# Performance work log

Hardware: AMD Instinct MI355X
Metric: run time of the kernel (lower is better)

## Reference

```python
import jax, jax.numpy as jnp
import numpy as np

DIM = 192
HEADS = 4
B, H, W = 4, 128, 128


def _dwconv3(x, w):
    # depthwise 3x3, padding=1: w has shape [C, 1, 3, 3], groups = C
    return jax.lax.conv_general_dilated(
        x, w, window_strides=(1, 1), padding='SAME',
        feature_group_count=x.shape[1],
        dimension_numbers=('NCHW', 'OIHW', 'NCHW'))


def _conv1x1(x, w):
    # w: [O, C] (squeezed 1x1 kernel), bias=False
    return jnp.einsum('bchw,oc->bohw', x, w)


def _l2norm(t):
    # torch F.normalize(dim=-1), eps=1e-12
    n = jnp.sqrt(jnp.sum(t * t, axis=-1, keepdims=True))
    return t / jnp.maximum(n, 1e-12)


def setup_inputs() -> dict:
    key = jax.random.key(0)
    ks = jax.random.split(key, 12)
    s = 0.05
    return {
        'x': jax.random.normal(ks[0], (B, DIM, H, W), jnp.float32),
        'x_hidden': jax.random.normal(ks[1], (B, DIM, H, W), jnp.float32),
        'qkv_w': jax.random.normal(ks[2], (3 * DIM, DIM), jnp.float32) * s,
        'qkv_dw_w': jax.random.normal(ks[3], (3 * DIM, 1, 3, 3), jnp.float32) * s,
        'q_mut_w': jax.random.normal(ks[4], (DIM, DIM), jnp.float32) * s,
        'q_mut_dw_w': jax.random.normal(ks[5], (DIM, 1, 3, 3), jnp.float32) * s,
        'kv_mut_w': jax.random.normal(ks[6], (2 * DIM, DIM), jnp.float32) * s,
        'kv_mut_dw_w': jax.random.normal(ks[7], (2 * DIM, 1, 3, 3), jnp.float32) * s,
        'proj_w': jax.random.normal(ks[8], (DIM, 2 * DIM), jnp.float32) * s,
        'temperature': jnp.ones((HEADS, 1, 1), jnp.float32),
        'temperature_mut': jnp.ones((HEADS, 1, 1), jnp.float32),
    }


def reference(x, x_hidden, qkv_w, qkv_dw_w, q_mut_w, q_mut_dw_w,
              kv_mut_w, kv_mut_dw_w, proj_w, temperature, temperature_mut):
    b, c, h, w = x.shape
    heads = HEADS

    qkv = _dwconv3(_conv1x1(x, qkv_w), qkv_dw_w)
    q, k, v = jnp.split(qkv, 3, axis=1)
    q_mut = _dwconv3(_conv1x1(x, q_mut_w), q_mut_dw_w)
    kv_mut = _dwconv3(_conv1x1(x_hidden, kv_mut_w), kv_mut_dw_w)
    k_mut, v_mut = jnp.split(kv_mut, 2, axis=1)

    def rs(t):  # b (head c') h w -> b head c' (h w)
        return t.reshape(b, heads, c // heads, h * w)

    q, k, v = rs(q), rs(k), rs(v)
    q_mut, k_mut, v_mut = rs(q_mut), rs(k_mut), rs(v_mut)

    q, k = _l2norm(q), _l2norm(k)
    q_mut, k_mut = _l2norm(q_mut), _l2norm(k_mut)

    # channel-wise (transposed) attention: [b, head, c', c']
    attn = jax.nn.softmax(
        jnp.einsum('bhcn,bhdn->bhcd', q, k) * temperature, axis=-1)
    cross = jax.nn.softmax(
        jnp.einsum('bhcn,bhdn->bhcd', q_mut, k_mut) * temperature_mut, axis=-1)

    out = jnp.einsum('bhcd,bhdn->bhcn', attn, v).reshape(b, c, h, w)
    out_mut = jnp.einsum('bhcd,bhdn->bhcn', cross, v_mut).reshape(b, c, h, w)

    return _conv1x1(jnp.concatenate((out, out_mut), axis=1), proj_w)
```

## Files before the change

### kernel.cpp

```cpp
#include <hip/hip_runtime.h>
#include <hip/hip_bf16.h>

typedef __hip_bfloat16 bf16;
using short8  = __attribute__((ext_vector_type(8))) short;
using float4_ = __attribute__((ext_vector_type(4))) float;

#define B_    4
#define C_    192
#define NN    16384
#define HEADS 4
#define CHD   48
#define TOT   1152

__device__ __forceinline__ float b2f(bf16 v) { return __bfloat162float(v); }
__device__ __forceinline__ float s2f(short s) {
    return __uint_as_float(((unsigned)(unsigned short)s) << 16);
}

__global__ __launch_bounds__(256) void kprep_w(
    const float* __restrict__ qkv_w, const float* __restrict__ qm_w,
    const float* __restrict__ kvm_w, bf16* __restrict__ Wb)
{
    int i = blockIdx.x * 256 + threadIdx.x;
    if (i >= TOT * C_) return;
    int r = i / C_, c = i % C_;
    float v = (r < 576) ? qkv_w[r * C_ + c]
            : (r < 768) ? qm_w[(r - 576) * C_ + c]
                        : kvm_w[(r - 768) * C_ + c];
    Wb[i] = __float2bfloat16(v);
}

__global__ __launch_bounds__(256) void kprep_x(
    const float* __restrict__ x, const float* __restrict__ xh,
    int p, bf16* __restrict__ Xt)
{
    const int pb = blockIdx.z >> 1, src = blockIdx.z & 1;
    const int b = p * 2 + pb;
    const float* in = (src == 0 ? x : xh) + (size_t)b * C_ * NN;
    bf16* outp = Xt + ((size_t)pb * 2 + src) * NN * C_;
    const int n0 = blockIdx.x * 64, c0 = blockIdx.y * 64;
    __shared__ float t[64][65];
    const int tid = threadIdx.x;

    #pragma unroll
    for (int it = 0; it < 4; ++it) {
        const int id = it * 256 + tid;
        const int c = id >> 4, i4 = (id & 15) * 4;
        const float4_ v = *(const float4_*)&in[(size_t)(c0 + c) * NN + n0 + i4];
        t[c][i4 + 0] = v[0]; t[c][i4 + 1] = v[1];
        t[c][i4 + 2] = v[2]; t[c][i4 + 3] = v[3];
    }
    __syncthreads();

    #pragma unroll
    for (int it = 0; it < 2; ++it) {
        const int id = it * 256 + tid;
        const int n = id >> 3, j8 = (id & 7) * 8;
        short8 sv;
        #pragma unroll
        for (int k = 0; k < 8; ++k) {
            bf16 h = __float2bfloat16(t[j8 + k][n]);
            sv[k] = *reinterpret_cast<short*>(&h);
        }
        *(short8*)&outp[(size_t)(n0 + n) * C_ + c0 + j8] = sv;
    }
}

__global__ __launch_bounds__(256) void kgemm(
    const bf16* __restrict__ Wb, const bf16* __restrict__ Xt,
    bf16* __restrict__ Y)
{
    const int nt0 = blockIdx.x * 128;
    const int mt0 = blockIdx.y * 64;
    const int pb  = blockIdx.z;
    const int tid = threadIdx.x;
    const bf16* Xs = Xt + ((size_t)pb * 2 + (mt0 >= 768 ? 1 : 0)) * NN * C_;
    bf16* Yp = Y + (size_t)pb * TOT * NN;

    __shared__ short sA[64][72];
    __shared__ short sB[128][72];

    const int wave = tid >> 6, lane = tid & 63;
    const int mw = (wave & 1) * 32, nw = (wave >> 1) * 64;
    const int lm = lane & 15, lq = lane >> 4;

    float4_ acc[2][4];
    #pragma unroll
    for (int i = 0; i < 2; ++i)
        #pragma unroll
        for (int j = 0; j < 4; ++j)
            acc[i][j] = (float4_){0.f, 0.f, 0.f, 0.f};

    for (int kc = 0; kc < 192; kc += 64) {
        __syncthreads();
        {
            int r = tid >> 3, c8 = (tid & 7) * 8;
            #pragma unroll
            for (int it = 0; it < 2; ++it, r += 32)
                *(short8*)&sA[r][c8] =
                    *(const short8*)&Wb[(size_t)(mt0 + r) * C_ + kc + c8];
        }
        {
            int r = tid >> 3, c8 = (tid & 7) * 8;
            #pragma unroll
            for (int it = 0; it < 4; ++it, r += 32)
                *(short8*)&sB[r][c8] =
                    *(const short8*)&Xs[(size_t)(nt0 + r) * C_ + kc + c8];
        }
        __syncthreads();
        #pragma unroll
        for (int kk = 0; kk < 64; kk += 32) {
            short8 af[2], bfr[4];
            const int ko = kk + lq * 8;
            #pragma unroll
            for (int i = 0; i < 2; ++i)
                af[i] = *(const short8*)&sA[mw + i * 16 + lm][ko];
            #pragma unroll
            for (int j = 0; j < 4; ++j)
                bfr[j] = *(const short8*)&sB[nw + j * 16 + lm][ko];
            #pragma unroll
            for (int i = 0; i < 2; ++i)
                #pragma unroll
                for (int j = 0; j < 4; ++j)
                    acc[i][j] = __builtin_amdgcn_mfma_f32_16x16x32_bf16(
                        af[i], bfr[j], acc[i][j], 0, 0, 0);
        }
    }
    #pragma unroll
    for (int i = 0; i < 2; ++i)
        #pragma unroll
        for (int j = 0; j < 4; ++j) {
            const int n = nt0 + nw + j * 16 + lm;
            #pragma unroll
            for (int r = 0; r < 4; ++r) {
                const int m = mt0 + mw + i * 16 + lq * 4 + r;
                Yp[(size_t)m * NN + n] = __float2bfloat16(acc[i][j][r]);
            }
        }
}

__device__ __forceinline__ void kdw_load_row(
    float* r, const bf16* __restrict__ Yc, int row, int x0, int lane)
{
    float f[8];
    if (row >= 0 && row <= 127) {
        short8 v = *(const short8*)(Yc + row * 128 + x0);
        #pragma unroll
        for (int i = 0; i < 8; ++i) f[i] = s2f(v[i]);
    } else {
        #pragma unroll
        for (int i = 0; i < 8; ++i) f[i] = 0.f;
    }
    const float lf = __shfl(f[7], lane - 1);
    const float rf = __shfl(f[0], lane + 1);
    r[0] = (x0 > 0)   ? lf : 0.f;
    r[9] = (x0 < 120) ? rf : 0.f;
    #pragma unroll
    for (int i = 0; i < 8; ++i) r[i + 1] = f[i];
}

__global__ __launch_bounds__(256) void kdw(
    const bf16* __restrict__ Y,
    const float* __restrict__ qkv_dw, const float* __restrict__ qm_dw,
    const float* __restrict__ kvm_dw, int p, bf16* __restrict__ QT,
    float* __restrict__ nrmsq)
{
    const int ch  = blockIdx.x;
    const int pb  = blockIdx.z;
    const int b   = p * 2 + pb;
    const int tid = threadIdx.x;
    const int tx = tid & 15, ty = tid >> 4;
    const int lane = tid & 63;
    const int x0 = tx * 8;
    const int y0 = blockIdx.y * 64 + ty * 4;

    const float* dwp = (ch < 576) ? qkv_dw + (size_t)ch * 9
                     : (ch < 768) ? qm_dw + (size_t)(ch - 576) * 9
                                  : kvm_dw + (size_t)(ch - 768) * 9;
    float w[9];
    #pragma unroll
    for (int i = 0; i < 9; ++i) w[i] = dwp[i];

    const bf16* Yc = Y + ((size_t)pb * TOT + ch) * NN;
    bf16* qout = QT + ((size_t)b * TOT + ch) * NN;

    float r0[10], r1[10], r2[10];
    kdw_load_row(r0, Yc, y0 - 1, x0, lane);
    kdw_load_row(r1, Yc, y0,     x0, lane);

    float ssq = 0.f;
    #pragma unroll
    for (int yy = 0; yy < 4; ++yy) {
        kdw_load_row(r2, Yc, y0 + yy + 1, x0, lane);
        short8 sv;
        #pragma unroll
        for (int xx = 0; xx < 8; ++xx) {
            float s = w[0] * r0[xx] + w[1] * r0[xx + 1] + w[2] * r0[xx + 2]
                    + w[3] * r1[xx] + w[4] * r1[xx + 1] + w[5] * r1[xx + 2]
                    + w[6] * r2[xx] + w[7] * r2[xx + 1] + w[8] * r2[xx + 2];
            ssq += s * s;
            bf16 h = __float2bfloat16(s);
            sv[xx] = *reinterpret_cast<short*>(&h);
        }
        *(short8*)&qout[(size_t)(y0 + yy) * 128 + x0] = sv;
        #pragma unroll
        for (int i = 0; i < 10; ++i) { r0[i] = r1[i]; r1[i] = r2[i]; }
    }

    int cls = -1, ci = 0;
    if (ch < 192)                    { cls = 0; ci = ch; }
    else if (ch < 384)               { cls = 1; ci = ch - 192; }
    else if (ch >= 576 && ch < 768)  { cls = 2; ci = ch - 576; }
    else if (ch >= 768 && ch < 960)  { cls = 3; ci = ch - 768; }
    if (cls >= 0) {
        #pragma unroll
        for (int off = 32; off > 0; off >>= 1) ssq += __shfl_down(ssq, off);
        __shared__ float red[4];
        if ((tid & 63) == 0) red[tid >> 6] = ssq;
        __syncthreads();
        if (tid == 0)
            atomicAdd(&nrmsq[(b * 4 + cls) * 192 + ci],
                      red[0] + red[1] + red[2] + red[3]);
    }
}

__global__ __launch_bounds__(256) void k3_mfma(
    const bf16* __restrict__ QT, float* __restrict__ Gpart)
{
    const int chunk = blockIdx.x;
    const int t = blockIdx.y >> 2, h = blockIdx.y & 3;
    const int b = blockIdx.z;
    const int qch = (t == 0 ? 0 : 576) + h * CHD;
    const int kch = (t == 0 ? 192 : 768) + h * CHD;
    const bf16* qp = QT + ((size_t)b * TOT + qch) * NN;
    const bf16* kp = QT + ((size_t)b * TOT + kch) * NN;

    const int tid = threadIdx.x;
    const int wave = tid >> 6, lane = tid & 63;
    const int lm = lane & 15, lq = lane >> 4;
    const int n0 = chunk * 512 + wave * 128;

    float4_ acc[3][3];
    #pragma unroll
    for (int i = 0; i < 3; ++i)
        #pragma unroll
        for (int j = 0; j < 3; ++j)
            acc[i][j] = (float4_){0.f, 0.f, 0.f, 0.f};

    #pragma unroll
    for (int kk = 0; kk < 128; kk += 32) {
        short8 af[3], bfr[3];
        const int ko = n0 + kk + lq * 8;
        #pragma unroll
        for (int i = 0; i < 3; ++i)
            af[i] = *(const short8*)&qp[(size_t)(i * 16 + lm) * NN + ko];
        #pragma unroll
        for (int j = 0; j < 3; ++j)
            bfr[j] = *(const short8*)&kp[(size_t)(j * 16 + lm) * NN + ko];
        #pragma unroll
        for (int i = 0; i < 3; ++i)
            #pragma unroll
            for (int j = 0; j < 3; ++j)
                acc[i][j] = __builtin_amdgcn_mfma_f32_16x16x32_bf16(
                    af[i], bfr[j], acc[i][j], 0, 0, 0);
    }

    __shared__ float sW[4][48 * 49];
    #pragma unroll
    for (int i = 0; i < 3; ++i)
        #pragma unroll
        for (int j = 0; j < 3; ++j)
            #pragma unroll
            for (int r = 0; r < 4; ++r)
                sW[wave][(i * 16 + lq * 4 + r) * 49 + j * 16 + lm] = acc[i][j][r];
    __syncthreads();

    const int gidx = ((t * 4 + b) * 4 + h);
    float* Gp = Gpart + ((size_t)gidx * 32 + chunk) * 2304;
    for (int idx = tid; idx < 2304; idx += 256) {
        const int c = idx / 48, d = idx % 48;
        Gp[idx] = sW[0][c * 49 + d] + sW[1][c * 49 + d]
                + sW[2][c * 49 + d] + sW[3][c * 49 + d];
    }
}

__global__ __launch_bounds__(256) void kred(
    const float* __restrict__ Gpart, float* __restrict__ G)
{
    const int idx = blockIdx.x * 256 + threadIdx.x;
    if (idx >= 32 * 2304) return;
    const int g = idx / 2304, i = idx % 2304;
    const float* p = Gpart + (size_t)g * 32 * 2304 + i;
    float s = 0.f;
    #pragma unroll
    for (int ch = 0; ch < 32; ++ch) s += p[(size_t)ch * 2304];
    G[(size_t)g * 2304 + i] = s;
}

__global__ __launch_bounds__(256) void k4a_softmax(
    const float* __restrict__ G, const float* __restrict__ nrmsq,
    const float* __restrict__ tq, const float* __restrict__ tm,
    float* __restrict__ P)
{
    const int gidx = blockIdx.x;
    const int h = gidx & 3, tb = gidx >> 2;
    const int b = tb & 3, t = tb >> 2;
    const float* Gp = G + (size_t)gidx * 2304;
    float* Pp = P + (size_t)gidx * 2304;

    const int tid = threadIdx.x;
    const int wave = tid >> 6, lane = tid & 63;
    const int clsq = (t == 0) ? 0 : 2, clsk = (t == 0) ? 1 : 3;
    const float tmp = (t == 0 ? tq[h] : tm[h]);

    float nk = 1.f;
    if (lane < 48)
        nk = fmaxf(sqrtf(fmaxf(nrmsq[(b * 4 + clsk) * 192 + h * 48 + lane], 0.f)),
                   1e-12f);
    const float sk = tmp / nk;

    const int c0 = blockIdx.y * 12 + wave * 3;
    #pragma unroll
    for (int cc = 0; cc < 3; ++cc) {
        const int c = c0 + cc;
        const float nq =
            fmaxf(sqrtf(fmaxf(nrmsq[(b * 4 + clsq) * 192 + h * 48 + c], 0.f)),
                  1e-12f);
        float L = -1e30f;
        if (lane < 48) L = Gp[c * 48 + lane] * sk / nq;
        float mx = L;
        #pragma unroll
        for (int off = 32; off > 0; off >>= 1)
            mx = fmaxf(mx, __shfl_xor(mx, off));
        float e = (lane < 48) ? expf(L - mx) : 0.f;
        float sum = e;
        #pragma unroll
        for (int off = 32; off > 0; off >>= 1)
            sum += __shfl_xor(sum, off);
        if (lane < 48) Pp[c * 48 + lane] = e / sum;
    }
}

__global__ __launch_bounds__(256) void k4b_fold(
    const float* __restrict__ P, const float* __restrict__ proj_w,
    bf16* __restrict__ Mb)
{
    const int gidx = blockIdx.x;
    const int h = gidx & 3, tb = gidx >> 2;
    const int b = tb & 3, t = tb >> 2;
    const int o0 = blockIdx.y * 48;
    const int colb = t * 192 + h * 48;

    __shared__ float sP[48][49];
    __shared__ float sW[48][49];
    const int tid = threadIdx.x;
    const float* Pp = P + (size_t)gidx * 2304;

    for (int idx = tid; idx < 2304; idx += 256) {
        const int r = idx / 48, q = idx % 48;
        sP[r][q] = Pp[idx];
        sW[r][q] = proj_w[(size_t)(o0 + r) * 384 + colb + q];
    }
    __syncthreads();

    for (int idx = tid; idx < 2304; idx += 256) {
        const int o = idx / 48, d = idx % 48;
        float s = 0.f;
        #pragma unroll
        for (int c = 0; c < 48; ++c) s += sW[o][c] * sP[c][d];
        Mb[((size_t)b * 192 + o0 + o) * 384 + colb + d] = __float2bfloat16(s);
    }
}

__global__ __launch_bounds__(512, 4) void k5_mfma(
    const bf16* __restrict__ Mb, const bf16* __restrict__ QT,
    float* __restrict__ out)
{
    const int nt0 = blockIdx.x * 128;
    const int b   = blockIdx.z;
    const int tid = threadIdx.x;

    __shared__ short sM[192][72];
    __shared__ short sB[128][72];

    const int wave = tid >> 6, lane = tid & 63;
    const int wm = (wave >> 2) * 96;
    const int wn = (wave & 3) * 32;
    const int lm = lane & 15, lq = lane >> 4;

    const bf16* Qb = QT + (size_t)b * TOT * NN;
    const bf16* Mp = Mb + (size_t)b * 192 * 384;

    float4_ acc[6][2];
    #pragma unroll
    for (int i = 0; i < 6; ++i)
        #pragma unroll
        for (int j = 0; j < 2; ++j)
            acc[i][j] = (float4_){0.f, 0.f, 0.f, 0.f};

    for (int kc = 0; kc < 384; kc += 64) {
        __syncthreads();
        #pragma unroll
        for (int it = 0; it < 3; ++it) {
            const int id = it * 512 + tid;
            const int r = id >> 3, g = (id & 7) * 8;
            *(short8*)&sM[r][g] =
                *(const short8*)&Mp[(size_t)r * 384 + kc + g];
        }
        const int chbase = (kc < 192) ? (384 + kc) : (960 + (kc - 192));
        #pragma unroll
        for (int it = 0; it < 2; ++it) {
            const int t = it * 512 + tid;
            const int d = t & 63, ng = t >> 6;
            short8 v = *(const short8*)
                &Qb[(size_t)(chbase + d) * NN + nt0 + ng * 8];
            #pragma unroll
            for (int j = 0; j < 8; ++j)
                sB[ng * 8 + j][d] = v[j];
        }
        __syncthreads();
        #pragma unroll
        for (int kk = 0; kk < 64; kk += 32) {
            short8 af[6], bfr[2];
            const int ko = kk + lq * 8;
            #pragma unroll
            for (int i = 0; i < 6; ++i)
                af[i] = *(const short8*)&sM[wm + i * 16 + lm][ko];
            #pragma unroll
            for (int j = 0; j < 2; ++j)
                bfr[j] = *(const short8*)&sB[wn + j * 16 + lm][ko];
            #pragma unroll
            for (int i = 0; i < 6; ++i)
                #pragma unroll
                for (int j = 0; j < 2; ++j)
                    acc[i][j] = __builtin_amdgcn_mfma_f32_16x16x32_bf16(
                        af[i], bfr[j], acc[i][j], 0, 0, 0);
        }
    }
    #pragma unroll
    for (int i = 0; i < 6; ++i)
        #pragma unroll
        for (int j = 0; j < 2; ++j) {
            const int n = nt0 + wn + j * 16 + lm;
            #pragma unroll
            for (int r = 0; r < 4; ++r) {
                const int m = wm + i * 16 + lq * 4 + r;
                out[((size_t)b * C_ + m) * NN + n] = acc[i][j][r];
            }
        }
}

extern "C" void kernel_launch(void* const* d_in, const int* in_sizes, int n_in,
                              void* d_out, int out_size, void* d_ws, size_t ws_size,
                              hipStream_t stream)
{
    const float* x     = (const float*)d_in[0];
    const float* xh    = (const float*)d_in[1];
    const float* qkvw  = (const float*)d_in[2];
    const float* qkvdw = (const float*)d_in[3];
    const float* qmw   = (const float*)d_in[4];
    const float* qmdw  = (const float*)d_in[5];
    const float* kvmw  = (const float*)d_in[6];
    const float* kvmdw = (const float*)d_in[7];
    const float* projw = (const float*)d_in[8];
    const float* tq    = (const float*)d_in[9];
    const float* tm    = (const float*)d_in[10];
    float* out = (float*)d_out;

    char* ws = (char*)d_ws;
    size_t off = 0;
    bf16*  QT = (bf16*)(ws + off);  off += (size_t)B_ * TOT * NN * 2;
    bf16*  Y  = (bf16*)(ws + off);  off += (size_t)2 * TOT * NN * 2;
    bf16*  Xt = (bf16*)(ws + off);  off += (size_t)2 * 2 * NN * C_ * 2;
    bf16*  Wb = (bf16*)(ws + off);  off += (size_t)TOT * C_ * 2;
    float* nrm = (float*)(ws + off); off += (size_t)B_ * 4 * 192 * 4;
    float* G   = (float*)(ws + off); off += (size_t)2 * B_ * HEADS * 48 * 48 * 4;
    bf16*  Mb  = (bf16*)(ws + off);  off += (size_t)B_ * 192 * 384 * 2;
    float* Gpart = (float*)(ws + off); off += (size_t)32 * 32 * 2304 * 4;
    float* P = Gpart;

    hipMemsetAsync(nrm, 0, (size_t)B_ * 4 * 192 * 4, stream);

    kprep_w<<<dim3((TOT * C_ + 255) / 256), 256, 0, stream>>>(qkvw, qmw, kvmw, Wb);

    for (int p = 0; p < 2; ++p) {
        kprep_x<<<dim3(256, 3, 4), 256, 0, stream>>>(x, xh, p, Xt);
        kgemm  <<<dim3(128, 18, 2), 256, 0, stream>>>(Wb, Xt, Y);
        kdw    <<<dim3(1152, 2, 2), 256, 0, stream>>>(Y, qkvdw, qmdw, kvmdw, p, QT, nrm);
    }

    k3_mfma    <<<dim3(32, 8, B_), 256, 0, stream>>>(QT, Gpart);
    kred       <<<dim3((32 * 2304 + 255) / 256), 256, 0, stream>>>(Gpart, G);
    k4a_softmax<<<dim3(32, 4), 256, 0, stream>>>(G, nrm, tq, tm, P);
    k4b_fold   <<<dim3(32, 4), 256, 0, stream>>>(P, projw, Mb);
    k5_mfma    <<<dim3(128, 1, B_), 512, 0, stream>>>(Mb, QT, out);
}
```

Measured before the change: 332.2 us.

## Fuse softmax with proj fold and make depthwise blocks cover full channel

Each depthwise-conv block now covers the whole 128x128 channel plane with 8 rows per thread, so the squared-norm sum can be written directly instead of accumulated atomically, which removes the memset. Softmax and the projection fold are merged into one kernel that keeps the probabilities in shared memory, saving a launch and a global round trip. The cost is fewer, larger blocks (32 for the fused kernel, 2304 for kdw) and less parallelism in those stages.

```diff
diff --git a/kernel.cpp b/kernel.cpp
--- a/kernel.cpp
+++ b/kernel.cpp
@@ -172,7 +172,7 @@
     const int tx = tid & 15, ty = tid >> 4;
     const int lane = tid & 63;
     const int x0 = tx * 8;
-    const int y0 = blockIdx.y * 64 + ty * 4;
+    const int y0 = ty * 8;
 
     const float* dwp = (ch < 576) ? qkv_dw + (size_t)ch * 9
                      : (ch < 768) ? qm_dw + (size_t)(ch - 576) * 9
@@ -190,7 +190,7 @@
 
     float ssq = 0.f;
     #pragma unroll
-    for (int yy = 0; yy < 4; ++yy) {
+    for (int yy = 0; yy < 8; ++yy) {
         kdw_load_row(r2, Yc, y0 + yy + 1, x0, lane);
         short8 sv;
         #pragma unroll
@@ -219,8 +219,8 @@
         if ((tid & 63) == 0) red[tid >> 6] = ssq;
         __syncthreads();
         if (tid == 0)
-            atomicAdd(&nrmsq[(b * 4 + cls) * 192 + ci],
-                      red[0] + red[1] + red[2] + red[3]);
+            nrmsq[(b * 4 + cls) * 192 + ci] =
+                red[0] + red[1] + red[2] + red[3];
     }
 }
 
@@ -297,32 +297,37 @@
     G[(size_t)g * 2304 + i] = s;
 }
 
-__global__ __launch_bounds__(256) void k4a_softmax(
+__global__ __launch_bounds__(256) void k4ab(
     const float* __restrict__ G, const float* __restrict__ nrmsq,
-    const float* __restrict__ tq, const float* __restrict__ tm,
-    float* __restrict__ P)
+    const float* __restrict__ proj_w, const float* __restrict__ tq,
+    const float* __restrict__ tm, bf16* __restrict__ Mb)
 {
     const int gidx = blockIdx.x;
     const int h = gidx & 3, tb = gidx >> 2;
     const int b = tb & 3, t = tb >> 2;
     const float* Gp = G + (size_t)gidx * 2304;
-    float* Pp = P + (size_t)gidx * 2304;
-
-    const int tid = threadIdx.x;
+    const int tid = threadIdx.x;
+    const int colb = t * 192 + h * 48;
+
+    __shared__ float sP[48][49];
+    __shared__ float sWp[192][49];
+
+    for (int idx = tid; idx < 192 * 48; idx += 256) {
+        const int o = idx / 48, c = idx % 48;
+        sWp[o][c] = proj_w[(size_t)o * 384 + colb + c];
+    }
+
     const int wave = tid >> 6, lane = tid & 63;
     const int clsq = (t == 0) ? 0 : 2, clsk = (t == 0) ? 1 : 3;
     const float tmp = (t == 0 ? tq[h] : tm[h]);
-
     float nk = 1.f;
     if (lane < 48)
         nk = fmaxf(sqrtf(fmaxf(nrmsq[(b * 4 + clsk) * 192 + h * 48 + lane], 0.f)),
                    1e-12f);
     const float sk = tmp / nk;
-
-    const int c0 = blockIdx.y * 12 + wave * 3;
-    #pragma unroll
-    for (int cc = 0; cc < 3; ++cc) {
-        const int c = c0 + cc;
+    #pragma unroll
+    for (int cc = 0; cc < 12; ++cc) {
+        const int c = wave * 12 + cc;
         const float nq =
             fmaxf(sqrtf(fmaxf(nrmsq[(b * 4 + clsq) * 192 + h * 48 + c], 0.f)),
                   1e-12f);
@@ -337,38 +342,16 @@
         #pragma unroll
         for (int off = 32; off > 0; off >>= 1)
             sum += __shfl_xor(sum, off);
-        if (lane < 48) Pp[c * 48 + lane] = e / sum;
-    }
-}
-
-__global__ __launch_bounds__(256) void k4b_fold(
-    const float* __restrict__ P, const float* __restrict__ proj_w,
-    bf16* __restrict__ Mb)
-{
-    const int gidx = blockIdx.x;
-    const int h = gidx & 3, tb = gidx >> 2;
-    const int b = tb & 3, t = tb >> 2;
-    const int o0 = blockIdx.y * 48;
-    const int colb = t * 192 + h * 48;
-
-    __shared__ float sP[48][49];
-    __shared__ float sW[48][49];
-    const int tid = threadIdx.x;
-    const float* Pp = P + (size_t)gidx * 2304;
-
-    for (int idx = tid; idx < 2304; idx += 256) {
-        const int r = idx / 48, q = idx % 48;
-        sP[r][q] = Pp[idx];
-        sW[r][q] = proj_w[(size_t)(o0 + r) * 384 + colb + q];
+        if (lane < 48) sP[c][lane] = e / sum;
     }
     __syncthreads();
 
-    for (int idx = tid; idx < 2304; idx += 256) {
+    for (int idx = tid; idx < 192 * 48; idx += 256) {
         const int o = idx / 48, d = idx % 48;
         float s = 0.f;
         #pragma unroll
-        for (int c = 0; c < 48; ++c) s += sW[o][c] * sP[c][d];
-        Mb[((size_t)b * 192 + o0 + o) * 384 + colb + d] = __float2bfloat16(s);
+        for (int c = 0; c < 48; ++c) s += sWp[o][c] * sP[c][d];
+        Mb[((size_t)b * 192 + o) * 384 + colb + d] = __float2bfloat16(s);
     }
 }
 
@@ -477,21 +460,17 @@
     float* G   = (float*)(ws + off); off += (size_t)2 * B_ * HEADS * 48 * 48 * 4;
     bf16*  Mb  = (bf16*)(ws + off);  off += (size_t)B_ * 192 * 384 * 2;
     float* Gpart = (float*)(ws + off); off += (size_t)32 * 32 * 2304 * 4;
-    float* P = Gpart;
-
-    hipMemsetAsync(nrm, 0, (size_t)B_ * 4 * 192 * 4, stream);
 
     kprep_w<<<dim3((TOT * C_ + 255) / 256), 256, 0, stream>>>(qkvw, qmw, kvmw, Wb);
 
     for (int p = 0; p < 2; ++p) {
         kprep_x<<<dim3(256, 3, 4), 256, 0, stream>>>(x, xh, p, Xt);
         kgemm  <<<dim3(128, 18, 2), 256, 0, stream>>>(Wb, Xt, Y);
-        kdw    <<<dim3(1152, 2, 2), 256, 0, stream>>>(Y, qkvdw, qmdw, kvmdw, p, QT, nrm);
-    }
-
-    k3_mfma    <<<dim3(32, 8, B_), 256, 0, stream>>>(QT, Gpart);
-    kred       <<<dim3((32 * 2304 + 255) / 256), 256, 0, stream>>>(Gpart, G);
-    k4a_softmax<<<dim3(32, 4), 256, 0, stream>>>(G, nrm, tq, tm, P);
-    k4b_fold   <<<dim3(32, 4), 256, 0, stream>>>(P, projw, Mb);
-    k5_mfma    <<<dim3(128, 1, B_), 512, 0, stream>>>(Mb, QT, out);
-}
+        kdw    <<<dim3(1152, 1, 2), 256, 0, stream>>>(Y, qkvdw, qmdw, kvmdw, p, QT, nrm);
+    }
+
+    k3_mfma<<<dim3(32, 8, B_), 256, 0, stream>>>(QT, Gpart);
+    kred   <<<dim3((32 * 2304 + 255) / 256), 256, 0, stream>>>(Gpart, G);
+    k4ab   <<<dim3(32), 256, 0, stream>>>(G, nrm, projw, tq, tm, Mb);
+    k5_mfma<<<dim3(128, 1, B_), 512, 0, stream>>>(Mb, QT, out);
+}
```

New measurement: 358.3 us. +7.9%, slower.
